# Kernel tuning notes

Hardware: AMD Instinct MI355X
Metric: run time of the kernel (lower is better)

Reference implementation:

```python
import jax, jax.numpy as jnp
import numpy as np

B, T, IN, H, OUT = 128, 256, 1, 5000, 20


def setup_inputs() -> dict:
    key = jax.random.key(0)
    k1, k2, k3, k4, k5 = jax.random.split(key, 5)
    return {
        "x": jax.random.normal(k1, (B, T, IN), dtype=jnp.float32),
        "W_in": jax.random.normal(k2, (H, IN), dtype=jnp.float32) * (1.0 / np.sqrt(IN)),
        "b_in": jax.random.normal(k3, (H,), dtype=jnp.float32) * 0.01,
        "W_out": jax.random.normal(k4, (OUT, H), dtype=jnp.float32) * (1.0 / np.sqrt(H)),
        "b_out": jax.random.normal(k5, (OUT,), dtype=jnp.float32) * 0.01,
    }


def reference(x, W_in, b_in, W_out, b_out):
    # x: [B, T, IN]; recurrence: h_{t+1} = tanh(x_t @ W_in^T + b_in + h_t)
    batch = x.shape[0]
    hidden = W_in.shape[0]
    h0 = jnp.zeros((batch, hidden), dtype=x.dtype)
    xs = jnp.swapaxes(x, 0, 1)  # [T, B, IN] for scan over time

    def step(h, x_t):
        h_new = jnp.tanh(x_t @ W_in.T + b_in + h)
        return h_new, None

    h_final, _ = jax.lax.scan(step, h0, xs)
    logits = h_final @ W_out.T + b_out  # [B, OUT]
    return jax.nn.softmax(logits, axis=-1)
```

## Files before the change

kernel.cpp:

```cpp
#include <hip/hip_runtime.h>

#define T_STEPS 256
#define BATCH   128
#define HIDDEN  5000
#define NHALF   2500
#define NOUT    20

__global__ __launch_bounds__(256)
void rnn_recurrence(const float* __restrict__ x,
                    const float* __restrict__ W_in,
                    const float* __restrict__ b_in,
                    float* __restrict__ h_out) {
    const int b  = blockIdx.y;
    const int i0 = blockIdx.x * 256 + threadIdx.x;
    if (i0 >= NHALF) return;
    const int i1 = i0 + NHALF;

    const float c     = 2.8853900817779268f;
    const float inv_c = 0.34657359027997264f;
    const float n2c   = -5.7707801635558537f;

    const float wc0 = W_in[i0] * c;
    const float wc1 = W_in[i1] * c;
    const float K0  = __builtin_amdgcn_exp2f(b_in[i0] * c);
    const float K1  = __builtin_amdgcn_exp2f(b_in[i1] * c);

    const float* __restrict__ xrow = x + b * T_STEPS;

    float hc0 = 0.0f, hc1 = 0.0f;
    #pragma unroll 16
    for (int t = 0; t < T_STEPS; ++t) {
        const float xv = xrow[t];
        float u0 = fmaf(xv, wc0, hc0);
        float u1 = fmaf(xv, wc1, hc1);
        float e0 = __builtin_amdgcn_exp2f(u0);
        float e1 = __builtin_amdgcn_exp2f(u1);
        float d0 = fmaf(e0, K0, 1.0f);
        float d1 = fmaf(e1, K1, 1.0f);
        float r0 = __builtin_amdgcn_rcpf(d0);
        float r1 = __builtin_amdgcn_rcpf(d1);
        hc0 = fmaf(r0, n2c, c);
        hc1 = fmaf(r1, n2c, c);
    }
    h_out[b * HIDDEN + i0] = hc0 * inv_c;
    h_out[b * HIDDEN + i1] = hc1 * inv_c;
}

__global__ __launch_bounds__(256)
void head_softmax(const float* __restrict__ h,
                  const float* __restrict__ W_out,
                  const float* __restrict__ b_out,
                  float* __restrict__ out) {
    const int b   = blockIdx.x;
    const int tid = threadIdx.x;

    const float4* __restrict__ h4 = (const float4*)(h + b * HIDDEN);
    const float4* __restrict__ w4 = (const float4*)W_out;

    float acc[NOUT];
    #pragma unroll
    for (int o = 0; o < NOUT; ++o) acc[o] = 0.0f;

    for (int i4 = tid; i4 < HIDDEN / 4; i4 += 256) {
        const float4 hv = h4[i4];
        #pragma unroll
        for (int o = 0; o < NOUT; ++o) {
            const float4 wv = w4[o * (HIDDEN / 4) + i4];
            acc[o] = fmaf(hv.x, wv.x, acc[o]);
            acc[o] = fmaf(hv.y, wv.y, acc[o]);
            acc[o] = fmaf(hv.z, wv.z, acc[o]);
            acc[o] = fmaf(hv.w, wv.w, acc[o]);
        }
    }

    #pragma unroll
    for (int o = 0; o < NOUT; ++o) {
        #pragma unroll
        for (int s = 32; s > 0; s >>= 1)
            acc[o] += __shfl_down(acc[o], s, 64);
    }

    __shared__ float partial[4][NOUT];
    const int wid = tid >> 6, lane = tid & 63;
    if (lane == 0) {
        #pragma unroll
        for (int o = 0; o < NOUT; ++o) partial[wid][o] = acc[o];
    }
    __syncthreads();

    if (tid == 0) {
        float logits[NOUT];
        float m = -1e30f;
        #pragma unroll
        for (int o = 0; o < NOUT; ++o) {
            float v = partial[0][o] + partial[1][o] + partial[2][o]
                    + partial[3][o] + b_out[o];
            logits[o] = v;
            m = fmaxf(m, v);
        }
        float s = 0.0f;
        float e[NOUT];
        #pragma unroll
        for (int o = 0; o < NOUT; ++o) {
            e[o] = __builtin_amdgcn_exp2f((logits[o] - m) * 1.4426950408889634f);
            s += e[o];
        }
        const float inv = 1.0f / s;
        #pragma unroll
        for (int o = 0; o < NOUT; ++o) out[b * NOUT + o] = e[o] * inv;
    }
}

extern "C" void kernel_launch(void* const* d_in, const int* in_sizes, int n_in,
                              void* d_out, int out_size, void* d_ws, size_t ws_size,
                              hipStream_t stream) {
    const float* x     = (const float*)d_in[0];
    const float* W_in  = (const float*)d_in[1];
    const float* b_in  = (const float*)d_in[2];
    const float* W_out = (const float*)d_in[3];
    const float* b_out = (const float*)d_in[4];
    float* out  = (float*)d_out;
    float* h_ws = (float*)d_ws;

    dim3 grid1((NHALF + 255) / 256, BATCH);
    rnn_recurrence<<<grid1, 256, 0, stream>>>(x, W_in, b_in, h_ws);
    head_softmax<<<BATCH, 256, 0, stream>>>(h_ws, W_out, b_out, out);
}
```

Measured before the change: 102.1 us.

## Fuse output projection into recurrence kernel with per-block partial logits

Each recurrence block now multiplies its final hidden values by W_out and reduces them into per-block partial logits, so the full hidden state is no longer written to and reread from global memory. A small second kernel sums the ten partials per batch row, adds the bias and applies softmax using wave shuffles. Out-of-range threads are kept alive with zeroed contributions so they can join the reductions. The cost is 20 W_out loads per thread and extra reductions inside the recurrence kernel, plus a second launch that stays on the critical path.

Result: faster. 97.83 us (-4.2%).

```diff
diff --git a/kernel.cpp b/kernel.cpp
--- a/kernel.cpp
+++ b/kernel.cpp
@@ -5,25 +5,29 @@
 #define HIDDEN  5000
 #define NHALF   2500
 #define NOUT    20
+#define NBLK    10
 
 __global__ __launch_bounds__(256)
-void rnn_recurrence(const float* __restrict__ x,
-                    const float* __restrict__ W_in,
-                    const float* __restrict__ b_in,
-                    float* __restrict__ h_out) {
-    const int b  = blockIdx.y;
-    const int i0 = blockIdx.x * 256 + threadIdx.x;
-    if (i0 >= NHALF) return;
-    const int i1 = i0 + NHALF;
+void rnn_fused(const float* __restrict__ x,
+               const float* __restrict__ W_in,
+               const float* __restrict__ b_in,
+               const float* __restrict__ W_out,
+               float* __restrict__ part) {
+    const int b   = blockIdx.y;
+    const int tid = threadIdx.x;
+    const int i0  = blockIdx.x * 256 + tid;
+    const bool valid = (i0 < NHALF);
+    const int j0 = valid ? i0 : 0;
+    const int j1 = j0 + NHALF;
 
     const float c     = 2.8853900817779268f;
     const float inv_c = 0.34657359027997264f;
     const float n2c   = -5.7707801635558537f;
 
-    const float wc0 = W_in[i0] * c;
-    const float wc1 = W_in[i1] * c;
-    const float K0  = __builtin_amdgcn_exp2f(b_in[i0] * c);
-    const float K1  = __builtin_amdgcn_exp2f(b_in[i1] * c);
+    const float wc0 = W_in[j0] * c;
+    const float wc1 = W_in[j1] * c;
+    const float K0  = __builtin_amdgcn_exp2f(b_in[j0] * c);
+    const float K1  = __builtin_amdgcn_exp2f(b_in[j1] * c);
 
     const float* __restrict__ xrow = x + b * T_STEPS;
 
@@ -42,35 +46,15 @@
         hc0 = fmaf(r0, n2c, c);
         hc1 = fmaf(r1, n2c, c);
     }
-    h_out[b * HIDDEN + i0] = hc0 * inv_c;
-    h_out[b * HIDDEN + i1] = hc1 * inv_c;
-}
-
-__global__ __launch_bounds__(256)
-void head_softmax(const float* __restrict__ h,
-                  const float* __restrict__ W_out,
-                  const float* __restrict__ b_out,
-                  float* __restrict__ out) {
-    const int b   = blockIdx.x;
-    const int tid = threadIdx.x;
-
-    const float4* __restrict__ h4 = (const float4*)(h + b * HIDDEN);
-    const float4* __restrict__ w4 = (const float4*)W_out;
+    const float h0 = valid ? hc0 * inv_c : 0.0f;
+    const float h1 = valid ? hc1 * inv_c : 0.0f;
 
     float acc[NOUT];
     #pragma unroll
-    for (int o = 0; o < NOUT; ++o) acc[o] = 0.0f;
-
-    for (int i4 = tid; i4 < HIDDEN / 4; i4 += 256) {
-        const float4 hv = h4[i4];
-        #pragma unroll
-        for (int o = 0; o < NOUT; ++o) {
-            const float4 wv = w4[o * (HIDDEN / 4) + i4];
-            acc[o] = fmaf(hv.x, wv.x, acc[o]);
-            acc[o] = fmaf(hv.y, wv.y, acc[o]);
-            acc[o] = fmaf(hv.z, wv.z, acc[o]);
-            acc[o] = fmaf(hv.w, wv.w, acc[o]);
-        }
+    for (int o = 0; o < NOUT; ++o) {
+        const float w0 = W_out[o * HIDDEN + j0];
+        const float w1 = W_out[o * HIDDEN + j1];
+        acc[o] = fmaf(h0, w0, h1 * w1);
     }
 
     #pragma unroll
@@ -80,35 +64,48 @@
             acc[o] += __shfl_down(acc[o], s, 64);
     }
 
-    __shared__ float partial[4][NOUT];
+    __shared__ float red[4][NOUT];
     const int wid = tid >> 6, lane = tid & 63;
     if (lane == 0) {
         #pragma unroll
-        for (int o = 0; o < NOUT; ++o) partial[wid][o] = acc[o];
+        for (int o = 0; o < NOUT; ++o) red[wid][o] = acc[o];
     }
     __syncthreads();
 
-    if (tid == 0) {
-        float logits[NOUT];
-        float m = -1e30f;
+    if (tid < NOUT) {
+        const float v = red[0][tid] + red[1][tid] + red[2][tid] + red[3][tid];
+        part[(b * NBLK + blockIdx.x) * NOUT + tid] = v;
+    }
+}
+
+__global__ __launch_bounds__(64)
+void softmax_head(const float* __restrict__ part,
+                  const float* __restrict__ b_out,
+                  float* __restrict__ out) {
+    const int b = blockIdx.x;
+    const int o = threadIdx.x;
+
+    float v = -1e30f;
+    if (o < NOUT) {
+        float s = b_out[o];
         #pragma unroll
-        for (int o = 0; o < NOUT; ++o) {
-            float v = partial[0][o] + partial[1][o] + partial[2][o]
-                    + partial[3][o] + b_out[o];
-            logits[o] = v;
-            m = fmaxf(m, v);
-        }
-        float s = 0.0f;
-        float e[NOUT];
-        #pragma unroll
-        for (int o = 0; o < NOUT; ++o) {
-            e[o] = __builtin_amdgcn_exp2f((logits[o] - m) * 1.4426950408889634f);
-            s += e[o];
-        }
-        const float inv = 1.0f / s;
-        #pragma unroll
-        for (int o = 0; o < NOUT; ++o) out[b * NOUT + o] = e[o] * inv;
+        for (int blk = 0; blk < NBLK; ++blk)
+            s += part[(b * NBLK + blk) * NOUT + o];
+        v = s;
     }
+
+    float m = v;
+    #pragma unroll
+    for (int s = 32; s > 0; s >>= 1) m = fmaxf(m, __shfl_xor(m, s, 64));
+
+    float e = (o < NOUT)
+            ? __builtin_amdgcn_exp2f((v - m) * 1.4426950408889634f)
+            : 0.0f;
+    float ssum = e;
+    #pragma unroll
+    for (int s = 32; s > 0; s >>= 1) ssum += __shfl_xor(ssum, s, 64);
+
+    if (o < NOUT) out[b * NOUT + o] = e / ssum;
 }
 
 extern "C" void kernel_launch(void* const* d_in, const int* in_sizes, int n_in,
@@ -120,9 +117,9 @@
     const float* W_out = (const float*)d_in[3];
     const float* b_out = (const float*)d_in[4];
     float* out  = (float*)d_out;
-    float* h_ws = (float*)d_ws;
+    float* part = (float*)d_ws;
 
-    dim3 grid1((NHALF + 255) / 256, BATCH);
-    rnn_recurrence<<<grid1, 256, 0, stream>>>(x, W_in, b_in, h_ws);
-    head_softmax<<<BATCH, 256, 0, stream>>>(h_ws, W_out, b_out, out);
+    dim3 grid1(NBLK, BATCH);
+    rnn_fused<<<grid1, 256, 0, stream>>>(x, W_in, b_in, W_out, part);
+    softmax_head<<<BATCH, 64, 0, stream>>>(part, b_out, out);
 }
```
